# Optimization experiments

Hardware: AMD Instinct MI355X
Metric: run time of the kernel (lower is better)

Reference implementation:

```python
import jax, jax.numpy as jnp
import numpy as np

TAU_MEM = 20.0
V_THRESH = 1.0
DECAY = float(np.exp(-1.0 / TAU_MEM))
SLOPE = 5.0  # fast-sigmoid surrogate slope


@jax.custom_vjp
def spike(x):
    # Heaviside spike with fast-sigmoid surrogate gradient
    return (x > 0).astype(x.dtype)

def _spike_fwd(x):
    return spike(x), x

def _spike_bwd(x, g):
    surr = 1.0 / (1.0 + SLOPE * jnp.abs(x)) ** 2
    return (g * surr,)

spike.defvjp(_spike_fwd, _spike_bwd)


def setup_inputs() -> dict:
    key = jax.random.key(0)
    k1, k2 = jax.random.split(key)
    B, T, n_in, n_out = 32, 1000, 1024, 512
    input_spikes_seq = (jax.random.uniform(k1, (B, T, n_in)) < 0.05).astype(jnp.float32)
    w_init_scale = 0.5
    W = jax.random.normal(k2, (n_out, n_in), dtype=jnp.float32) * (w_init_scale / np.sqrt(n_in))
    return {"input_spikes_seq": input_spikes_seq, "W": W}


def reference(input_spikes_seq, W):
    # input_spikes_seq: (B, T, n_in); W: (n_out, n_in) -> out: (B, T, n_out)
    B, T, _ = input_spikes_seq.shape
    n_out = W.shape[0]
    # Hoist the GEMM out of the time loop: (B,T,n_in) x (n_out,n_in) -> (B,T,n_out)
    I = jnp.einsum('bti,oi->bto', input_spikes_seq, W)
    I_t = jnp.transpose(I, (1, 0, 2))  # (T, B, n_out)

    def step(v, i_t):
        v = v * DECAY + i_t
        s = spike(v - V_THRESH)
        v = v * (1.0 - jax.lax.stop_gradient(s))  # reset, detached as in torch
        return v, s

    v0 = jnp.zeros((B, n_out), dtype=input_spikes_seq.dtype)
    _, out_t = jax.lax.scan(step, v0, I_t)  # out_t: (T, B, n_out)
    return jnp.transpose(out_t, (1, 0, 2))
```

## Files before the change

kernel.cpp:

```cpp
#include <hip/hip_runtime.h>


#define N_IN   1024
#define N_OUT  512
#define DECAY_F 0.95122942450071400910f
#define SCALE     67108864.0
#define SCALE_INV 1.4901161193847656e-08f

typedef int  v4i  __attribute__((ext_vector_type(4)));
typedef int  v16i __attribute__((ext_vector_type(16)));

typedef __attribute__((address_space(1))) const void gv_t;
typedef __attribute__((address_space(3))) void lv_t;
__device__ __forceinline__ void gl16(const signed char* g, signed char* l) {
    __builtin_amdgcn_global_load_lds((gv_t*)g, (lv_t*)l, 16, 0, 0);
}

__global__ __launch_bounds__(256) void prep(const float* __restrict__ S,
                                            signed char* __restrict__ S8,
                                            const float* __restrict__ W,
                                            signed char* __restrict__ D8,
                                            int nS16blocks) {
    if ((int)blockIdx.x < nS16blocks) {
        const int g = blockIdx.x * 256 + threadIdx.x;
        const float4* p = reinterpret_cast<const float4*>(S) + (size_t)g * 4;
        union { signed char c[16]; int4 v; } u;
#pragma unroll
        for (int q = 0; q < 4; ++q) {
            const float4 v = p[q];
            u.c[q * 4 + 0] = (signed char)(v.x != 0.f);
            u.c[q * 4 + 1] = (signed char)(v.y != 0.f);
            u.c[q * 4 + 2] = (signed char)(v.z != 0.f);
            u.c[q * 4 + 3] = (signed char)(v.w != 0.f);
        }
        reinterpret_cast<int4*>(S8)[g] = u.v;
    } else {
        const int n  = blockIdx.x - nS16blocks;
        const int k0 = threadIdx.x * 4;
        const float4 wv = *reinterpret_cast<const float4*>(W + (size_t)n * N_IN + k0);
        const float ww[4] = {wv.x, wv.y, wv.z, wv.w};
        int pk[3] = {0, 0, 0};
#pragma unroll
        for (int j = 0; j < 4; ++j) {
            long long wi = (long long)rint((double)ww[j] * SCALE);
            const int d0 = (int)((wi + 128) & 255) - 128; wi = (wi - d0) >> 8;
            const int d1 = (int)((wi + 128) & 255) - 128; wi = (wi - d1) >> 8;
            const int d2 = (int)wi;
            pk[0] |= (d0 & 255) << (8 * j);
            pk[1] |= (d1 & 255) << (8 * j);
            pk[2] |= (d2 & 255) << (8 * j);
        }
#pragma unroll
        for (int d = 0; d < 3; ++d)
            *reinterpret_cast<int*>(D8 + (size_t)(d * N_OUT + n) * N_IN + k0) = pk[d];
    }
}

#define BM 128
#define BN 64
#define BK 64
#define ATILE (BM * BK)
#define BTILE (192 * BK)
#define BUFSZ (ATILE + BTILE)

#define BARRIER __builtin_amdgcn_s_barrier()
#define SB0 __builtin_amdgcn_sched_barrier(0)
#define LGKM(n) do { asm volatile("s_waitcnt lgkmcnt(" #n ")" ::: "memory"); SB0; } while (0)
#define VMCNT_(n) asm volatile("s_waitcnt vmcnt(" #n ")" ::: "memory")
#define LDV(off) (*reinterpret_cast<const v4i*>(lds + (off)))
#define MFMA_I8 __builtin_amdgcn_mfma_i32_32x32x32_i8

__global__ __launch_bounds__(256, 2) void gemm_i8(
        const signed char* __restrict__ S8,
        const signed char* __restrict__ D8,
        float* __restrict__ I, int M) {
    extern __shared__ signed char lds[];

    const int tid  = threadIdx.x;
    const int lane = tid & 63;
    const int w    = tid >> 6;
    const int wwm  = w >> 1;
    const int wwn  = w & 1;

    const int nwx = (M / BM) * (N_OUT / BN) / 8;
    const int u   = (blockIdx.x & 7) * nwx + (blockIdx.x >> 3);
    const int bm  = u >> 3;
    const int bn  = u & 7;
    const int m0 = bm * BM;
    const int n0 = bn * BN;

    const int lrow  = lane >> 2;
    const int sslot = (lane & 3) << 4;
    const int swzs  = ((lrow >> 1) & 3) << 4;
    const int scola = sslot ^ swzs;
    const int srw   = w * 16 + lrow;

    const signed char* aSrc0 = S8 + (size_t)(m0 + srw) * N_IN + scola;
    const signed char* aSrc1 = aSrc0 + (size_t)64 * N_IN;
    const signed char* bS0 = D8 + (size_t)(0 * N_OUT + n0 + srw) * N_IN + scola;
    const signed char* bS1 = D8 + (size_t)(1 * N_OUT + n0 + srw) * N_IN + scola;
    const signed char* bS2 = D8 + (size_t)(2 * N_OUT + n0 + srw) * N_IN + scola;

    const int aDst0 = srw * 64 - (lrow * 64 + sslot) + (w * 16) * 64;
    const int aD0 = (w * 16) * 64;
    const int aD1 = aD0 + 64 * 64;
    const int bD0 = ATILE + (0 * 64 + w * 16) * 64;
    const int bD1 = ATILE + (1 * 64 + w * 16) * 64;
    const int bD2 = ATILE + (2 * 64 + w * 16) * 64;
    (void)aDst0;

    v16i acc[2][3];
#pragma unroll
    for (int mf = 0; mf < 2; ++mf)
#pragma unroll
        for (int d = 0; d < 3; ++d)
#pragma unroll
            for (int i = 0; i < 16; ++i) acc[mf][d][i] = 0;

    const int fr = lane & 31;
    const int kh = (lane >> 5) * 16;
    const int swzr = ((fr >> 1) & 3) << 4;
    const int kx0 = kh ^ swzr;
    const int kx1 = (32 + kh) ^ swzr;
    const int ra0 = (wwm * 64 + fr) * 64;
    const int ra1 = (wwm * 64 + 32 + fr) * 64;
    const int rb0 = ATILE + (0 * 64 + wwn * 32 + fr) * 64;
    const int rb1 = ATILE + (1 * 64 + wwn * 32 + fr) * 64;
    const int rb2 = ATILE + (2 * 64 + wwn * 32 + fr) * 64;

#define STAGE(STG, KT) do {                                                       \
        gl16(aSrc0 + (KT) * BK, lds + (STG) * BUFSZ + aD0);                       \
        gl16(aSrc1 + (KT) * BK, lds + (STG) * BUFSZ + aD1);                       \
        gl16(bS0 + (KT) * BK, lds + (STG) * BUFSZ + bD0);                         \
        gl16(bS1 + (KT) * BK, lds + (STG) * BUFSZ + bD1);                         \
        gl16(bS2 + (KT) * BK, lds + (STG) * BUFSZ + bD2);                         \
    } while (0)

#define TILE_STEP(CUR, STG, KT, DOSTAGE)                                          \
    {                                                                             \
        const int base = (CUR) * BUFSZ;                                           \
        v4i xa0, xa1, xb0, xb1, xb2;                                              \
        v4i ya0, ya1, yb0, yb1, yb2;                                              \
        xa0 = LDV(base + ra0 + kx0);                                              \
        xa1 = LDV(base + ra1 + kx0);                                              \
        xb0 = LDV(base + rb0 + kx0);                                              \
        xb1 = LDV(base + rb1 + kx0);                                              \
        xb2 = LDV(base + rb2 + kx0);                                              \
        SB0;                                                                      \
        ya0 = LDV(base + ra0 + kx1);                                              \
        ya1 = LDV(base + ra1 + kx1);                                              \
        yb0 = LDV(base + rb0 + kx1);                                              \
        yb1 = LDV(base + rb1 + kx1);                                              \
        yb2 = LDV(base + rb2 + kx1);                                              \
        SB0;                                                                      \
        LGKM(5);                                                                  \
        if (DOSTAGE) {                                                            \
            gl16(aSrc0 + (KT + 2) * BK, lds + (STG) * BUFSZ + aD0);               \
            gl16(aSrc1 + (KT + 2) * BK, lds + (STG) * BUFSZ + aD1);               \
        }                                                                         \
        __builtin_amdgcn_s_setprio(1);                                            \
        acc[0][0] = MFMA_I8(xa0, xb0, acc[0][0], 0, 0, 0);                        \
        acc[1][0] = MFMA_I8(xa1, xb0, acc[1][0], 0, 0, 0);                        \
        acc[0][1] = MFMA_I8(xa0, xb1, acc[0][1], 0, 0, 0);                        \
        acc[1][1] = MFMA_I8(xa1, xb1, acc[1][1], 0, 0, 0);                        \
        acc[0][2] = MFMA_I8(xa0, xb2, acc[0][2], 0, 0, 0);                        \
        acc[1][2] = MFMA_I8(xa1, xb2, acc[1][2], 0, 0, 0);                        \
        __builtin_amdgcn_s_setprio(0);                                            \
        if (DOSTAGE) {                                                            \
            gl16(bS0 + (KT + 2) * BK, lds + (STG) * BUFSZ + bD0);                 \
            gl16(bS1 + (KT + 2) * BK, lds + (STG) * BUFSZ + bD1);                 \
            gl16(bS2 + (KT + 2) * BK, lds + (STG) * BUFSZ + bD2);                 \
        }                                                                         \
        LGKM(0);                                                                  \
        __builtin_amdgcn_s_setprio(1);                                            \
        acc[0][0] = MFMA_I8(ya0, yb0, acc[0][0], 0, 0, 0);                        \
        acc[1][0] = MFMA_I8(ya1, yb0, acc[1][0], 0, 0, 0);                        \
        acc[0][1] = MFMA_I8(ya0, yb1, acc[0][1], 0, 0, 0);                        \
        acc[1][1] = MFMA_I8(ya1, yb1, acc[1][1], 0, 0, 0);                        \
        acc[0][2] = MFMA_I8(ya0, yb2, acc[0][2], 0, 0, 0);                        \
        acc[1][2] = MFMA_I8(ya1, yb2, acc[1][2], 0, 0, 0);                        \
        __builtin_amdgcn_s_setprio(0);                                            \
        if (DOSTAGE) { VMCNT_(5); } else { VMCNT_(0); }                           \
        BARRIER;                                                                  \
    }

    STAGE(0, 0);
    STAGE(1, 1);
    VMCNT_(5);
    BARRIER;

    TILE_STEP(0, 2, 0,  1)
    TILE_STEP(1, 0, 1,  1)
    TILE_STEP(2, 1, 2,  1)
    TILE_STEP(0, 2, 3,  1)
    TILE_STEP(1, 0, 4,  1)
    TILE_STEP(2, 1, 5,  1)
    TILE_STEP(0, 2, 6,  1)
    TILE_STEP(1, 0, 7,  1)
    TILE_STEP(2, 1, 8,  1)
    TILE_STEP(0, 2, 9,  1)
    TILE_STEP(1, 0, 10, 1)
    TILE_STEP(2, 1, 11, 1)
    TILE_STEP(0, 2, 12, 1)
    TILE_STEP(1, 0, 13, 1)
    TILE_STEP(2, 1, 14, 0)
    TILE_STEP(0, 0, 15, 0)

    const int col = fr;
    const int rb_ = (lane >> 5) * 4;
#pragma unroll
    for (int mf = 0; mf < 2; ++mf) {
#pragma unroll
        for (int reg = 0; reg < 16; ++reg) {
            const int row = (reg & 3) + 8 * (reg >> 2) + rb_;
            const long long v =
                ((long long)acc[mf][2][reg] << 16) +
                ((long long)acc[mf][1][reg] << 8) + (long long)acc[mf][0][reg];
            I[(size_t)(m0 + wwm * 64 + mf * 32 + row) * N_OUT + n0 + wwn * 32 + col] =
                (float)v * SCALE_INV;
        }
    }
}
#undef STAGE
#undef TILE_STEP

#define UT 50
__global__ __launch_bounds__(64) void lif_scan3(float* __restrict__ IO, int T) {
    const int idx = blockIdx.x * 64 + threadIdx.x;
    const int b = idx >> 9, o = idx & (N_OUT - 1);
    float* p = IO + (size_t)b * T * N_OUT + o;
    float ca[UT], cb[UT];
    float v = 0.f;
#pragma unroll
    for (int j = 0; j < UT; ++j) ca[j] = p[(size_t)j * N_OUT];
#pragma unroll 1
    for (int t0 = 0; t0 < T; t0 += 2 * UT) {
        if (t0 + UT < T) {
#pragma unroll
            for (int j = 0; j < UT; ++j) cb[j] = p[(size_t)(t0 + UT + j) * N_OUT];
        }
#pragma unroll
        for (int j = 0; j < UT; ++j) {
            v = v * DECAY_F + ca[j];
            float s = (v > 1.0f) ? 1.0f : 0.f;
            v *= (1.f - s);
            ca[j] = s;
        }
#pragma unroll
        for (int j = 0; j < UT; ++j) p[(size_t)(t0 + j) * N_OUT] = ca[j];
        if (t0 + UT >= T) break;
        if (t0 + 2 * UT < T) {
#pragma unroll
            for (int j = 0; j < UT; ++j) ca[j] = p[(size_t)(t0 + 2 * UT + j) * N_OUT];
        }
#pragma unroll
        for (int j = 0; j < UT; ++j) {
            v = v * DECAY_F + cb[j];
            float s = (v > 1.0f) ? 1.0f : 0.f;
            v *= (1.f - s);
            cb[j] = s;
        }
#pragma unroll
        for (int j = 0; j < UT; ++j) p[(size_t)(t0 + UT + j) * N_OUT] = cb[j];
    }
}

__global__ __launch_bounds__(256) void transpose_w(const float* __restrict__ W,
                                                   float* __restrict__ WT) {
    __shared__ float t[32][33];
    const int k0 = blockIdx.x * 32;
    const int n0 = blockIdx.y * 32;
    const int lx = threadIdx.x & 31;
    const int ly = threadIdx.x >> 5;
#pragma unroll
    for (int r = ly; r < 32; r += 8)
        t[r][lx] = W[(size_t)(n0 + r) * N_IN + k0 + lx];
    __syncthreads();
#pragma unroll
    for (int r = ly; r < 32; r += 8)
        WT[(size_t)(k0 + r) * N_OUT + n0 + lx] = t[lx][r];
}

__global__ __launch_bounds__(256) void gather_rows(
        const float* __restrict__ S, const float* __restrict__ WT,
        float* __restrict__ I, int M) {
    const int wid  = blockIdx.x * 4 + (threadIdx.x >> 6);
    const int lane = threadIdx.x & 63;
    if (wid >= M) return;
    const float* srow = S + (size_t)wid * N_IN;
    float4 a0 = {0.f, 0.f, 0.f, 0.f};
    float4 a1 = {0.f, 0.f, 0.f, 0.f};
    float sv[16];
#pragma unroll
    for (int g = 0; g < 16; ++g) sv[g] = srow[g * 64 + lane];
#pragma unroll
    for (int g = 0; g < 16; ++g) {
        unsigned long long m = __ballot(sv[g] != 0.0f);
        while (m) {
            const int bb = __builtin_ctzll(m);
            m &= m - 1;
            const int k = g * 64 + bb;
            const float* wp = WT + (size_t)k * N_OUT + lane * 4;
            const float4 w0 = *reinterpret_cast<const float4*>(wp);
            const float4 w1 = *reinterpret_cast<const float4*>(wp + 256);
            a0.x += w0.x; a0.y += w0.y; a0.z += w0.z; a0.w += w0.w;
            a1.x += w1.x; a1.y += w1.y; a1.z += w1.z; a1.w += w1.w;
        }
    }
    float* op = I + (size_t)wid * N_OUT + lane * 4;
    *reinterpret_cast<float4*>(op) = a0;
    *reinterpret_cast<float4*>(op + 256) = a1;
}

extern "C" void kernel_launch(void* const* d_in, const int* in_sizes, int n_in,
                              void* d_out, int out_size, void* d_ws, size_t ws_size,
                              hipStream_t stream) {
    const float* S = (const float*)d_in[0];
    const float* W = (const float*)d_in[1];
    float* out = (float*)d_out;

    const int K = N_IN;
    const int M = in_sizes[0] / K;
    const int B = 32;
    const int T = M / B;

    const size_t s8_bytes = (size_t)M * N_IN;
    const size_t d8_bytes = (size_t)3 * N_OUT * N_IN;
    const size_t need = s8_bytes + d8_bytes;

    if (ws_size >= need && (M % BM) == 0 && ((M / BM) * (N_OUT / BN)) % 8 == 0) {
        signed char* S8 = (signed char*)d_ws;
        signed char* D8 = (signed char*)d_ws + s8_bytes;
        const int nS16blocks = (M * N_IN / 16) / 256;
        prep<<<nS16blocks + N_OUT, 256, 0, stream>>>(S, S8, W, D8, nS16blocks);
        const size_t lds_bytes = (size_t)3 * BUFSZ;
        gemm_i8<<<(M / BM) * (N_OUT / BN), 256, lds_bytes, stream>>>(S8, D8, out, M);
        lif_scan3<<<(B * N_OUT) / 64, 64, 0, stream>>>(out, T);
    } else if (ws_size >= (size_t)N_IN * N_OUT * sizeof(float) && (M % 4) == 0) {
        float* WT = (float*)d_ws;
        dim3 tg(N_IN / 32, N_OUT / 32);
        transpose_w<<<tg, 256, 0, stream>>>(W, WT);
        gather_rows<<<M / 4, 256, 0, stream>>>(S, WT, out, M);
        lif_scan3<<<(B * N_OUT) / 64, 64, 0, stream>>>(out, T);
    }
}
```

Baseline: 128.3 us.

## Switch GEMM to double-buffered LDS pipeline with three blocks per CU

The int8 GEMM drops from a triple-buffered LDS ring with prefetch two tiles ahead to a double buffer with prefetch one tile ahead. Each step now waits for all outstanding global loads (vmcnt 0) before the barrier. LDS per block shrinks from 3 to 2 buffers and launch bounds move from 2 to 3 blocks per CU to raise occupancy. The trade is a shorter prefetch distance, so more global-load latency is exposed per block, and the intent is for the extra resident blocks to hide it.

```diff
diff --git a/kernel.cpp b/kernel.cpp
--- a/kernel.cpp
+++ b/kernel.cpp
@@ -70,7 +70,7 @@
 #define LDV(off) (*reinterpret_cast<const v4i*>(lds + (off)))
 #define MFMA_I8 __builtin_amdgcn_mfma_i32_32x32x32_i8
 
-__global__ __launch_bounds__(256, 2) void gemm_i8(
+__global__ __launch_bounds__(256, 3) void gemm_i8(
         const signed char* __restrict__ S8,
         const signed char* __restrict__ D8,
         float* __restrict__ I, int M) {
@@ -101,13 +101,11 @@
     const signed char* bS1 = D8 + (size_t)(1 * N_OUT + n0 + srw) * N_IN + scola;
     const signed char* bS2 = D8 + (size_t)(2 * N_OUT + n0 + srw) * N_IN + scola;
 
-    const int aDst0 = srw * 64 - (lrow * 64 + sslot) + (w * 16) * 64;
     const int aD0 = (w * 16) * 64;
     const int aD1 = aD0 + 64 * 64;
     const int bD0 = ATILE + (0 * 64 + w * 16) * 64;
     const int bD1 = ATILE + (1 * 64 + w * 16) * 64;
     const int bD2 = ATILE + (2 * 64 + w * 16) * 64;
-    (void)aDst0;
 
     v16i acc[2][3];
 #pragma unroll
@@ -136,9 +134,10 @@
         gl16(bS2 + (KT) * BK, lds + (STG) * BUFSZ + bD2);                         \
     } while (0)
 
-#define TILE_STEP(CUR, STG, KT, DOSTAGE)                                          \
+#define TILE_STEP(CUR, KT, DOSTAGE)                                               \
     {                                                                             \
         const int base = (CUR) * BUFSZ;                                           \
+        const int stg  = ((CUR) ^ 1);                                             \
         v4i xa0, xa1, xb0, xb1, xb2;                                              \
         v4i ya0, ya1, yb0, yb1, yb2;                                              \
         xa0 = LDV(base + ra0 + kx0);                                              \
@@ -147,6 +146,7 @@
         xb1 = LDV(base + rb1 + kx0);                                              \
         xb2 = LDV(base + rb2 + kx0);                                              \
         SB0;                                                                      \
+        if (DOSTAGE) STAGE(stg, KT + 1);                                          \
         ya0 = LDV(base + ra0 + kx1);                                              \
         ya1 = LDV(base + ra1 + kx1);                                              \
         yb0 = LDV(base + rb0 + kx1);                                              \
@@ -154,10 +154,6 @@
         yb2 = LDV(base + rb2 + kx1);                                              \
         SB0;                                                                      \
         LGKM(5);                                                                  \
-        if (DOSTAGE) {                                                            \
-            gl16(aSrc0 + (KT + 2) * BK, lds + (STG) * BUFSZ + aD0);               \
-            gl16(aSrc1 + (KT + 2) * BK, lds + (STG) * BUFSZ + aD1);               \
-        }                                                                         \
         __builtin_amdgcn_s_setprio(1);                                            \
         acc[0][0] = MFMA_I8(xa0, xb0, acc[0][0], 0, 0, 0);                        \
         acc[1][0] = MFMA_I8(xa1, xb0, acc[1][0], 0, 0, 0);                        \
@@ -166,11 +162,6 @@
         acc[0][2] = MFMA_I8(xa0, xb2, acc[0][2], 0, 0, 0);                        \
         acc[1][2] = MFMA_I8(xa1, xb2, acc[1][2], 0, 0, 0);                        \
         __builtin_amdgcn_s_setprio(0);                                            \
-        if (DOSTAGE) {                                                            \
-            gl16(bS0 + (KT + 2) * BK, lds + (STG) * BUFSZ + bD0);                 \
-            gl16(bS1 + (KT + 2) * BK, lds + (STG) * BUFSZ + bD1);                 \
-            gl16(bS2 + (KT + 2) * BK, lds + (STG) * BUFSZ + bD2);                 \
-        }                                                                         \
         LGKM(0);                                                                  \
         __builtin_amdgcn_s_setprio(1);                                            \
         acc[0][0] = MFMA_I8(ya0, yb0, acc[0][0], 0, 0, 0);                        \
@@ -180,31 +171,30 @@
         acc[0][2] = MFMA_I8(ya0, yb2, acc[0][2], 0, 0, 0);                        \
         acc[1][2] = MFMA_I8(ya1, yb2, acc[1][2], 0, 0, 0);                        \
         __builtin_amdgcn_s_setprio(0);                                            \
-        if (DOSTAGE) { VMCNT_(5); } else { VMCNT_(0); }                           \
+        VMCNT_(0);                                                                \
         BARRIER;                                                                  \
     }
 
     STAGE(0, 0);
-    STAGE(1, 1);
-    VMCNT_(5);
+    VMCNT_(0);
     BARRIER;
 
-    TILE_STEP(0, 2, 0,  1)
-    TILE_STEP(1, 0, 1,  1)
-    TILE_STEP(2, 1, 2,  1)
-    TILE_STEP(0, 2, 3,  1)
-    TILE_STEP(1, 0, 4,  1)
-    TILE_STEP(2, 1, 5,  1)
-    TILE_STEP(0, 2, 6,  1)
-    TILE_STEP(1, 0, 7,  1)
-    TILE_STEP(2, 1, 8,  1)
-    TILE_STEP(0, 2, 9,  1)
-    TILE_STEP(1, 0, 10, 1)
-    TILE_STEP(2, 1, 11, 1)
-    TILE_STEP(0, 2, 12, 1)
-    TILE_STEP(1, 0, 13, 1)
-    TILE_STEP(2, 1, 14, 0)
-    TILE_STEP(0, 0, 15, 0)
+    TILE_STEP(0, 0,  1)
+    TILE_STEP(1, 1,  1)
+    TILE_STEP(0, 2,  1)
+    TILE_STEP(1, 3,  1)
+    TILE_STEP(0, 4,  1)
+    TILE_STEP(1, 5,  1)
+    TILE_STEP(0, 6,  1)
+    TILE_STEP(1, 7,  1)
+    TILE_STEP(0, 8,  1)
+    TILE_STEP(1, 9,  1)
+    TILE_STEP(0, 10, 1)
+    TILE_STEP(1, 11, 1)
+    TILE_STEP(0, 12, 1)
+    TILE_STEP(1, 13, 1)
+    TILE_STEP(0, 14, 1)
+    TILE_STEP(1, 15, 0)
 
     const int col = fr;
     const int rb_ = (lane >> 5) * 4;
@@ -333,7 +323,7 @@
         signed char* D8 = (signed char*)d_ws + s8_bytes;
         const int nS16blocks = (M * N_IN / 16) / 256;
         prep<<<nS16blocks + N_OUT, 256, 0, stream>>>(S, S8, W, D8, nS16blocks);
-        const size_t lds_bytes = (size_t)3 * BUFSZ;
+        const size_t lds_bytes = (size_t)2 * BUFSZ;
         gemm_i8<<<(M / BM) * (N_OUT / BN), 256, lds_bytes, stream>>>(S8, D8, out, M);
         lif_scan3<<<(B * N_OUT) / 64, 64, 0, stream>>>(out, T);
     } else if (ws_size >= (size_t)N_IN * N_OUT * sizeof(float) && (M % 4) == 0) {
```

Result: no change. 128.8 us (+0.4%).
